# Kernel optimization log

Measured on AMD Instinct MI355X. Metric: run time of the kernel, lower is better.

## Reference

```python
import jax, jax.numpy as jnp
import numpy as np

B, C, O, H, W = 4, 256, 256, 64, 64
KH = KW = 3
KK = KH * KW
PAD = 1  # stride=1, padding=1 -> output spatial == input spatial


def setup_inputs() -> dict:
    key = jax.random.key(0)
    k0, k1, k2, k3 = jax.random.split(key, 4)
    x = jax.random.normal(k0, (B, C, H, W), jnp.float32)
    # offset-predicting conv: small weights -> realistic sub-pixel offsets
    w_off = jax.random.normal(k1, (3 * KK, C, KH, KW), jnp.float32) * 0.01
    b_off = jnp.zeros((3 * KK,), jnp.float32)
    w_def = jax.random.normal(k2, (O, C, KH, KW), jnp.float32) * (1.0 / np.sqrt(C * KK))
    b_def = jax.random.normal(k3, (O,), jnp.float32) * 0.01
    return {"x": x, "w_off": w_off, "b_off": b_off, "w_def": w_def, "b_def": b_def}


def _conv2d(x, w, b):
    y = jax.lax.conv_general_dilated(
        x, w, window_strides=(1, 1), padding=((PAD, PAD), (PAD, PAD)),
        dimension_numbers=("NCHW", "OIHW", "NCHW"))
    return y + b[None, :, None, None]


def _deform_conv2d(x, offsets, mask, w, b):
    # torchvision modulated DeformConv2d, stride=1, pad=1, dilation=1.
    Bx, Cx, Hx, Wx = x.shape
    Ox = w.shape[0]
    # offsets: [B, 2*KK, H, W] with channel 2k = dy, 2k+1 = dx for tap k
    off = offsets.reshape(Bx, KK, 2, Hx, Wx)
    ky, kx = jnp.meshgrid(jnp.arange(KH), jnp.arange(KW), indexing="ij")
    ky = ky.reshape(KK)
    kx = kx.reshape(KK)
    base_y = (ky[:, None, None] - PAD + jnp.arange(Hx)[None, :, None]).astype(x.dtype)  # [KK,H,1]
    base_x = (kx[:, None, None] - PAD + jnp.arange(Wx)[None, None, :]).astype(x.dtype)  # [KK,1,W]
    sy = off[:, :, 0] + base_y  # [B,KK,H,W] sample rows
    sx = off[:, :, 1] + base_x  # [B,KK,H,W] sample cols

    y0 = jnp.floor(sy)
    x0 = jnp.floor(sx)
    ty = sy - y0  # fractional weights (grad flows to offsets through these)
    tx = sx - x0

    x_flat = x.reshape(Bx, Cx, Hx * Wx)
    val = jnp.zeros((Bx, Cx, KK, Hx, Wx), x.dtype)
    for dy in (0, 1):  # 4 bilinear corners (fixed small loop)
        for dx in (0, 1):
            yi = y0.astype(jnp.int32) + dy
            xi = x0.astype(jnp.int32) + dx
            wgt = (ty if dy else 1.0 - ty) * (tx if dx else 1.0 - tx)
            valid = (yi >= 0) & (yi < Hx) & (xi >= 0) & (xi < Wx)  # zero outside
            idx = (jnp.clip(yi, 0, Hx - 1) * Wx + jnp.clip(xi, 0, Wx - 1)).reshape(Bx, 1, -1)
            g = jnp.take_along_axis(x_flat, idx, axis=2).reshape(Bx, Cx, KK, Hx, Wx)
            val = val + g * jnp.where(valid, wgt, 0.0)[:, None]

    val = val * mask.reshape(Bx, 1, KK, Hx, Wx)  # modulation
    out = jnp.einsum("bckhw,ock->bohw", val, w.reshape(Ox, Cx, KK))
    return out + b[None, :, None, None]


def reference(x, w_off, b_off, w_def, b_def):
    pred = _conv2d(x, w_off, b_off)            # [B, 3*KK, H, W]
    offsets = pred[:, : 2 * KK]                # [B, 2*KK, H, W]
    mask = jax.nn.sigmoid(pred[:, 2 * KK:])    # [B, KK, H, W]
    return _deform_conv2d(x, offsets, mask, w_def, b_def)
```

## Files before the change

### kernel.cpp

```cpp
#include <hip/hip_runtime.h>

#define BB 4
#define CCH 256
#define OCH 256
#define HH 64
#define WW 64
#define HWSZ 4096

typedef __bf16 bf16_t;
typedef bf16_t bf16x8 __attribute__((ext_vector_type(8)));
typedef float f32x4 __attribute__((ext_vector_type(4)));

__device__ __forceinline__ unsigned int bpack(float a, float b) {
    unsigned int ua = __float_as_uint(a);
    ua = (ua + 0x7FFFu + ((ua >> 16) & 1u)) >> 16;
    unsigned int ub = __float_as_uint(b);
    ub = (ub + 0x7FFFu + ((ub >> 16) & 1u)) >> 16;
    return ua | (ub << 16);
}
__device__ __forceinline__ float blo(unsigned int u) { return __uint_as_float(u << 16); }
__device__ __forceinline__ float bhi(unsigned int u) { return __uint_as_float(u & 0xFFFF0000u); }

__global__ __launch_bounds__(256) void k_xT(const float* __restrict__ x,
                                            ushort* __restrict__ xT) {
    int b = blockIdx.x >> 6;
    int h = blockIdx.x & 63;
    int tid = threadIdx.x;
    int wv = tid >> 6;
    int lane = tid & 63;

    __shared__ unsigned int buf[64][130];

    const float* xp = x + ((size_t)b * CCH + wv * 64) * HWSZ + h * WW + lane;
#pragma unroll 8
    for (int i = 0; i < 32; ++i) {
        float a = xp[(size_t)(2 * i) * HWSZ];
        float c = xp[(size_t)(2 * i + 1) * HWSZ];
        buf[lane][wv * 32 + i] = bpack(a, c);
    }
    __syncthreads();

    ushort* dst = xT + ((size_t)(b * 64 + h) * 64) * 256;
#pragma unroll
    for (int r = 0; r < 16; ++r) {
        int idx = tid + r * 256;
        int w = idx >> 6;
        int q = idx & 63;
        uint2 v = *(const uint2*)&buf[w][2 * q];
        *(uint2*)(dst + (size_t)w * 256 + q * 4) = v;
    }
}

__global__ void k_prep(const float* __restrict__ w_off, const float* __restrict__ w_def,
                       const float* __restrict__ b_def,
                       ushort* __restrict__ w1F, ushort* __restrict__ w2F,
                       float* __restrict__ P, float* __restrict__ out) {
    int i = blockIdx.x * blockDim.x + threadIdx.x;
    if (i < 73728) {
        int j = i & 7;
        int o = (i >> 3) & 31;
        int cSub = (i >> 8) & 31;
        int k = i >> 13;
        float v = 0.0f;
        if (o < 27) v = w_off[((size_t)o * CCH + cSub * 8 + j) * 9 + k];
        unsigned int u = __float_as_uint(v);
        u = (u + 0x7FFFu + ((u >> 16) & 1u)) >> 16;
        w1F[i] = (ushort)u;
        return;
    }
    i -= 73728;
    if (i < 589824) {
        int j = i & 7;
        int o = (i >> 3) & 255;
        int cg = (i >> 11) & 31;
        int k = i >> 16;
        float v = w_def[(size_t)o * 2304 + (cg * 8 + j) * 9 + k];
        unsigned int u = __float_as_uint(v);
        u = (u + 0x7FFFu + ((u >> 16) & 1u)) >> 16;
        w2F[i] = (ushort)u;
        return;
    }
    i -= 589824;
    if (i < 110592) {
        ((float4*)P)[i] = make_float4(0.f, 0.f, 0.f, 0.f);
        return;
    }
    i -= 110592;
    if (i < 1048576) {
        float v = b_def[(i >> 10) & 255];
        ((float4*)out)[i] = make_float4(v, v, v, v);
    }
}

__global__ __launch_bounds__(256) void k_pred3(const ushort* __restrict__ xT,
                                               const ushort* __restrict__ w1F,
                                               float* __restrict__ P) {
    int bid = blockIdx.x;
    int L = (bid & 7) * 128 + (bid >> 3);
    int g = L & 3;
    int h = (L >> 2) & 63;
    int b = L >> 8;
    int tid = threadIdx.x;
    int spx  = tid & 63;
    int sgrp = tid >> 6;
    int lane = tid & 63;
    int wv   = tid >> 6;
    int l16  = lane & 15;
    int lq   = lane >> 4;

    __shared__ ushort b_lds[2][4][4][16][8];

    const ushort* xTb = xT + (size_t)b * HWSZ * 256;
    const bf16x8* w1v = (const bf16x8*)w1F;

    f32x4 acc[2];
    acc[0] = (f32x4){0.f, 0.f, 0.f, 0.f};
    acc[1] = (f32x4){0.f, 0.f, 0.f, 0.f};

    auto stage = [&](int t, int buf) {
        int cg = 2 * g + (t >= 9);
        int k = t - (t >= 9 ? 9 : 0);
        int y   = h + k / 3 - 1;
        int pxs = spx + k % 3 - 1;
        bool ok = (y >= 0 && y < HH && pxs >= 0 && pxs < WW);
        uint4 v = make_uint4(0u, 0u, 0u, 0u);
        if (ok) v = *(const uint4*)(xTb + (size_t)(y * WW + pxs) * 256 + cg * 32 + sgrp * 8);
        *(uint4*)&b_lds[buf][sgrp][spx >> 4][spx & 15][0] = v;
    };

    stage(0, 0);
    __syncthreads();

    for (int t = 0; t < 18; ++t) {
        int cur = t & 1;
        int cg = 2 * g + (t >= 9);
        int k  = t - (t >= 9 ? 9 : 0);
        int row = k * 32 + cg * 4 + lq;
        bf16x8 a0 = w1v[(size_t)row * 32 + 0 * 16 + l16];
        bf16x8 a1 = w1v[(size_t)row * 32 + 1 * 16 + l16];
        if (t < 17) stage(t + 1, cur ^ 1);
        bf16x8 bfrag = *(const bf16x8*)&b_lds[cur][lq][wv][l16][0];
        acc[0] = __builtin_amdgcn_mfma_f32_16x16x32_bf16(a0, bfrag, acc[0], 0, 0, 0);
        acc[1] = __builtin_amdgcn_mfma_f32_16x16x32_bf16(a1, bfrag, acc[1], 0, 0, 0);
        __syncthreads();
    }

#pragma unroll
    for (int mf = 0; mf < 2; ++mf) {
#pragma unroll
        for (int r = 0; r < 4; ++r) {
            int o = mf * 16 + lq * 4 + r;
            if (o < 27) {
                atomicAdd(&P[((size_t)b * 27 + o) * HWSZ + h * WW + wv * 16 + l16],
                          acc[mf][r]);
            }
        }
    }
}

__global__ __launch_bounds__(512, 4) void k_deform8(const ushort* __restrict__ xT,
                                                    const float* __restrict__ P,
                                                    const float* __restrict__ b_off,
                                                    const ushort* __restrict__ w2F,
                                                    float* __restrict__ out) {
    int bid = blockIdx.x;
    int L = (bid & 7) * 64 + (bid >> 3);
    int cs = L & 1;
    int h  = (L >> 1) & 63;
    int b  = L >> 7;
    int tid = threadIdx.x;
    int lane = tid & 63;
    int wv   = tid >> 6;
    int l16  = lane & 15;
    int lq   = lane >> 4;
    int px   = tid >> 3;
    int cl   = tid & 7;

    __shared__ ushort b_lds[2][8][4][16][8];

    const char* xTc = (const char*)xT + (size_t)b * HWSZ * 512 + cs * 256 + cl * 16;
    const bf16x8* w2b = (const bf16x8*)w2F + (size_t)(cs * 16) * 256 + wv * 32 + l16;

    uint4* wdst0 = (uint4*)&b_lds[0][cl][px >> 4][(px & 15) ^ cl][0];
    uint4* wdst1 = (uint4*)&b_lds[1][cl][px >> 4][(px & 15) ^ cl][0];

    f32x4 acc[2][4];
#pragma unroll
    for (int mf = 0; mf < 2; ++mf)
#pragma unroll
        for (int nt = 0; nt < 4; ++nt) acc[mf][nt] = (f32x4){0.f, 0.f, 0.f, 0.f};

    const float* Pb = P + (size_t)b * 27 * HWSZ + h * WW + px;

    float pOy, pOx, pMr, bOy, bOx, bMr;
    float wgt[4];
    const char* aptr[4];

    auto loadP = [&](int k) {
        pOy = Pb[(size_t)(2 * k) * HWSZ];
        pOx = Pb[(size_t)(2 * k + 1) * HWSZ];
        pMr = Pb[(size_t)(18 + k) * HWSZ];
        bOy = b_off[2 * k];
        bOx = b_off[2 * k + 1];
        bMr = b_off[18 + k];
    };
    auto calcDesc = [&](int k) {
        float offy = pOy + bOy;
        float offx = pOx + bOx;
        float m = 1.0f / (1.0f + expf(-(pMr + bMr)));
        float sy = offy + (float)(h + k / 3 - 1);
        float sx = offx + (float)(px + k % 3 - 1);
        float y0f = floorf(sy), x0f = floorf(sx);
        float ty = sy - y0f, tx = sx - x0f;
        int y0 = (int)y0f, x0 = (int)x0f;
#pragma unroll
        for (int dy = 0; dy < 2; ++dy) {
#pragma unroll
            for (int dx = 0; dx < 2; ++dx) {
                int yi = y0 + dy, xi = x0 + dx;
                bool ok = (yi >= 0 && yi < HH && xi >= 0 && xi < WW);
                float wg = (dy ? ty : 1.0f - ty) * (dx ? tx : 1.0f - tx) * m;
                wgt[dy * 2 + dx]  = ok ? wg : 0.0f;
                aptr[dy * 2 + dx] = xTc + (size_t)(ok ? (yi * WW + xi) : 0) * 512;
            }
        }
    };

    uint4 gbA[4], gbB[4];
    float wgtA[4], wgtB[4];
    bf16x8 aA[2][2], aB[2][2];

    auto issueGatherTo = [&](uint4 (&gb)[4], float (&wg)[4], int off) {
#pragma unroll
        for (int c = 0; c < 4; ++c) gb[c] = *(const uint4*)(aptr[c] + off);
#pragma unroll
        for (int c = 0; c < 4; ++c) wg[c] = wgt[c];
    };
    auto combineFrom = [&](const uint4 (&g)[4], const float (&w)[4]) -> uint4 {
        uint4 r;
        {
            float lo = w[0]*blo(g[0].x) + w[1]*blo(g[1].x) + w[2]*blo(g[2].x) + w[3]*blo(g[3].x);
            float hi = w[0]*bhi(g[0].x) + w[1]*bhi(g[1].x) + w[2]*bhi(g[2].x) + w[3]*bhi(g[3].x);
            r.x = bpack(lo, hi);
        }
        {
            float lo = w[0]*blo(g[0].y) + w[1]*blo(g[1].y) + w[2]*blo(g[2].y) + w[3]*blo(g[3].y);
            float hi = w[0]*bhi(g[0].y) + w[1]*bhi(g[1].y) + w[2]*bhi(g[2].y) + w[3]*bhi(g[3].y);
            r.y = bpack(lo, hi);
        }
        {
            float lo = w[0]*blo(g[0].z) + w[1]*blo(g[1].z) + w[2]*blo(g[2].z) + w[3]*blo(g[3].z);
            float hi = w[0]*bhi(g[0].z) + w[1]*bhi(g[1].z) + w[2]*bhi(g[2].z) + w[3]*bhi(g[3].z);
            r.z = bpack(lo, hi);
        }
        {
            float lo = w[0]*blo(g[0].w) + w[1]*blo(g[1].w) + w[2]*blo(g[2].w) + w[3]*blo(g[3].w);
            float hi = w[0]*bhi(g[0].w) + w[1]*bhi(g[1].w) + w[2]*bhi(g[2].w) + w[3]*bhi(g[3].w);
            r.w = bpack(lo, hi);
        }
        return r;
    };
    auto loadATo = [&](bf16x8 (&a)[2][2], int t) {
        size_t base = ((size_t)((t >> 1) * 32 + (t & 1) * 8) + lq) * 256;
#pragma unroll
        for (int g = 0; g < 2; ++g)
#pragma unroll
            for (int mf = 0; mf < 2; ++mf)
                a[mf][g] = w2b[base + (size_t)g * 1024 + mf * 16];
    };

#define MFMA_BODY(BUF, AREG)                                                        \
    do {                                                                            \
        bf16x8 bfr[2][4];                                                           \
        _Pragma("unroll")                                                           \
        for (int g = 0; g < 2; ++g) {                                               \
            int kg = g * 4 + lq;                                                    \
            _Pragma("unroll")                                                       \
            for (int nt = 0; nt < 4; ++nt)                                          \
                bfr[g][nt] = *(const bf16x8*)&b_lds[BUF][kg][nt][l16 ^ kg][0];      \
        }                                                                           \
        _Pragma("unroll")                                                           \
        for (int g = 0; g < 2; ++g)                                                 \
            _Pragma("unroll")                                                       \
            for (int mf = 0; mf < 2; ++mf)                                          \
                _Pragma("unroll")                                                   \
                for (int nt = 0; nt < 4; ++nt)                                      \
                    acc[mf][nt] = __builtin_amdgcn_mfma_f32_16x16x32_bf16(          \
                        AREG[mf][g], bfr[g][nt], acc[mf][nt], 0, 0, 0);             \
    } while (0)

    loadP(0);
    calcDesc(0);
    issueGatherTo(gbA, wgtA, 0);
    issueGatherTo(gbB, wgtB, 128);
    loadP(1);
    loadATo(aA, 0);
    *wdst0 = combineFrom(gbA, wgtA);
    __syncthreads();

    for (int tp = 0; tp < 9; ++tp) {
        if (tp < 8) {
            calcDesc(tp + 1);
            issueGatherTo(gbA, wgtA, 0);
        }
        loadATo(aB, 2 * tp + 1);
        MFMA_BODY(0, aA);
        *wdst1 = combineFrom(gbB, wgtB);
        __syncthreads();

        if (tp < 8) {
            issueGatherTo(gbB, wgtB, 128);
            if (tp < 7) loadP(tp + 2);
            loadATo(aA, 2 * tp + 2);
        }
        MFMA_BODY(1, aB);
        if (tp < 8) {
            *wdst0 = combineFrom(gbA, wgtA);
        }
        __syncthreads();
    }
#undef MFMA_BODY

#pragma unroll
    for (int mf = 0; mf < 2; ++mf) {
#pragma unroll
        for (int nt = 0; nt < 4; ++nt) {
#pragma unroll
            for (int r = 0; r < 4; ++r) {
                int o = wv * 32 + mf * 16 + lq * 4 + r;
                atomicAdd(&out[((size_t)b * OCH + o) * HWSZ + h * WW + nt * 16 + l16],
                          acc[mf][nt][r]);
            }
        }
    }
}

extern "C" void kernel_launch(void* const* d_in, const int* in_sizes, int n_in,
                              void* d_out, int out_size, void* d_ws, size_t ws_size,
                              hipStream_t stream) {
    const float* x     = (const float*)d_in[0];
    const float* w_off = (const float*)d_in[1];
    const float* b_off = (const float*)d_in[2];
    const float* w_def = (const float*)d_in[3];
    const float* b_def = (const float*)d_in[4];
    float* out = (float*)d_out;

    float*  P   = (float*)d_ws;
    ushort* w1F = (ushort*)(P + (size_t)BB * 27 * HWSZ);
    ushort* w2F = w1F + 73728;
    ushort* xT  = w2F + 589824;

    hipLaunchKernelGGL(k_prep, dim3(7120), dim3(256), 0, stream,
                       w_off, w_def, b_def, w1F, w2F, P, out);
    hipLaunchKernelGGL(k_xT, dim3(BB * HH), dim3(256), 0, stream, x, xT);
    hipLaunchKernelGGL(k_pred3, dim3(1024), dim3(256), 0, stream, xT, w1F, P);
    hipLaunchKernelGGL(k_deform8, dim3(512), dim3(512), 0, stream, xT, P, b_off, w2F, out);
}
```

Measured before the change: 89.90 us.

## Merge transpose into prep kernel, use hardware bf16 convert, lighter barriers

Folds the x-transpose kernel into the prep kernel as its first 256 blocks, removing one launch. Replaces the manual bit-twiddling bf16 rounding with the compiler's native bf16 conversion. Swaps __syncthreads for a barrier that waits only on LDS counters, so global loads in flight are not drained. Reorders the pipelines so the global gather is issued before the MFMAs and the LDS store comes after (pred) or before (deform). The lighter barrier relies on no global-memory ordering being needed across it, and the native convert may round NaN or other edge cases differently.

```diff
diff --git a/kernel.cpp b/kernel.cpp
--- a/kernel.cpp
+++ b/kernel.cpp
@@ -9,53 +9,65 @@
 
 typedef __bf16 bf16_t;
 typedef bf16_t bf16x8 __attribute__((ext_vector_type(8)));
+typedef bf16_t bf16x2_t __attribute__((ext_vector_type(2)));
 typedef float f32x4 __attribute__((ext_vector_type(4)));
 
-__device__ __forceinline__ unsigned int bpack(float a, float b) {
-    unsigned int ua = __float_as_uint(a);
-    ua = (ua + 0x7FFFu + ((ua >> 16) & 1u)) >> 16;
-    unsigned int ub = __float_as_uint(b);
-    ub = (ub + 0x7FFFu + ((ub >> 16) & 1u)) >> 16;
-    return ua | (ub << 16);
+__device__ __forceinline__ unsigned int packbf(float a, float b) {
+    bf16x2_t p;
+    p.x = (__bf16)a;
+    p.y = (__bf16)b;
+    return __builtin_bit_cast(unsigned int, p);
 }
 __device__ __forceinline__ float blo(unsigned int u) { return __uint_as_float(u << 16); }
 __device__ __forceinline__ float bhi(unsigned int u) { return __uint_as_float(u & 0xFFFF0000u); }
 
-__global__ __launch_bounds__(256) void k_xT(const float* __restrict__ x,
-                                            ushort* __restrict__ xT) {
-    int b = blockIdx.x >> 6;
-    int h = blockIdx.x & 63;
-    int tid = threadIdx.x;
-    int wv = tid >> 6;
-    int lane = tid & 63;
-
-    __shared__ unsigned int buf[64][130];
-
-    const float* xp = x + ((size_t)b * CCH + wv * 64) * HWSZ + h * WW + lane;
+__device__ __forceinline__ void block_sync() {
+    asm volatile("s_waitcnt lgkmcnt(0)" ::: "memory");
+    __builtin_amdgcn_s_barrier();
+    __builtin_amdgcn_sched_barrier(0);
+}
+
+__global__ __launch_bounds__(256) void k_prep(const float* __restrict__ x,
+                                              const float* __restrict__ w_off,
+                                              const float* __restrict__ w_def,
+                                              const float* __restrict__ b_def,
+                                              ushort* __restrict__ xT,
+                                              ushort* __restrict__ w1F,
+                                              ushort* __restrict__ w2F,
+                                              float* __restrict__ P,
+                                              float* __restrict__ out) {
+    int bid = blockIdx.x;
+    if (bid < 256) {
+        int b = bid >> 6;
+        int h = bid & 63;
+        int tid = threadIdx.x;
+        int wv = tid >> 6;
+        int lane = tid & 63;
+
+        __shared__ unsigned int buf[64][130];
+
+        const float* xp = x + ((size_t)b * CCH + wv * 64) * HWSZ + h * WW + lane;
 #pragma unroll 8
-    for (int i = 0; i < 32; ++i) {
-        float a = xp[(size_t)(2 * i) * HWSZ];
-        float c = xp[(size_t)(2 * i + 1) * HWSZ];
-        buf[lane][wv * 32 + i] = bpack(a, c);
-    }
-    __syncthreads();
-
-    ushort* dst = xT + ((size_t)(b * 64 + h) * 64) * 256;
-#pragma unroll
-    for (int r = 0; r < 16; ++r) {
-        int idx = tid + r * 256;
-        int w = idx >> 6;
-        int q = idx & 63;
-        uint2 v = *(const uint2*)&buf[w][2 * q];
-        *(uint2*)(dst + (size_t)w * 256 + q * 4) = v;
-    }
-}
-
-__global__ void k_prep(const float* __restrict__ w_off, const float* __restrict__ w_def,
-                       const float* __restrict__ b_def,
-                       ushort* __restrict__ w1F, ushort* __restrict__ w2F,
-                       float* __restrict__ P, float* __restrict__ out) {
-    int i = blockIdx.x * blockDim.x + threadIdx.x;
+        for (int i = 0; i < 32; ++i) {
+            float a = xp[(size_t)(2 * i) * HWSZ];
+            float c = xp[(size_t)(2 * i + 1) * HWSZ];
+            buf[lane][wv * 32 + i] = packbf(a, c);
+        }
+        __syncthreads();
+
+        ushort* dst = xT + ((size_t)(b * 64 + h) * 64) * 256;
+#pragma unroll
+        for (int r = 0; r < 16; ++r) {
+            int idx = tid + r * 256;
+            int w = idx >> 6;
+            int q = idx & 63;
+            uint2 v = *(const uint2*)&buf[w][2 * q];
+            *(uint2*)(dst + (size_t)w * 256 + q * 4) = v;
+        }
+        return;
+    }
+
+    int i = (bid - 256) * 256 + threadIdx.x;
     if (i < 73728) {
         int j = i & 7;
         int o = (i >> 3) & 31;
@@ -63,9 +75,7 @@
         int k = i >> 13;
         float v = 0.0f;
         if (o < 27) v = w_off[((size_t)o * CCH + cSub * 8 + j) * 9 + k];
-        unsigned int u = __float_as_uint(v);
-        u = (u + 0x7FFFu + ((u >> 16) & 1u)) >> 16;
-        w1F[i] = (ushort)u;
+        w1F[i] = (ushort)(packbf(v, 0.f) & 0xFFFFu);
         return;
     }
     i -= 73728;
@@ -75,9 +85,7 @@
         int cg = (i >> 11) & 31;
         int k = i >> 16;
         float v = w_def[(size_t)o * 2304 + (cg * 8 + j) * 9 + k];
-        unsigned int u = __float_as_uint(v);
-        u = (u + 0x7FFFu + ((u >> 16) & 1u)) >> 16;
-        w2F[i] = (ushort)u;
+        w2F[i] = (ushort)(packbf(v, 0.f) & 0xFFFFu);
         return;
     }
     i -= 589824;
@@ -117,7 +125,7 @@
     acc[0] = (f32x4){0.f, 0.f, 0.f, 0.f};
     acc[1] = (f32x4){0.f, 0.f, 0.f, 0.f};
 
-    auto stage = [&](int t, int buf) {
+    auto stageLoad = [&](int t) -> uint4 {
         int cg = 2 * g + (t >= 9);
         int k = t - (t >= 9 ? 9 : 0);
         int y   = h + k / 3 - 1;
@@ -125,24 +133,32 @@
         bool ok = (y >= 0 && y < HH && pxs >= 0 && pxs < WW);
         uint4 v = make_uint4(0u, 0u, 0u, 0u);
         if (ok) v = *(const uint4*)(xTb + (size_t)(y * WW + pxs) * 256 + cg * 32 + sgrp * 8);
+        return v;
+    };
+    auto stageWrite = [&](uint4 v, int buf) {
         *(uint4*)&b_lds[buf][sgrp][spx >> 4][spx & 15][0] = v;
     };
 
-    stage(0, 0);
-    __syncthreads();
+    {
+        uint4 g0 = stageLoad(0);
+        stageWrite(g0, 0);
+    }
+    block_sync();
 
     for (int t = 0; t < 18; ++t) {
         int cur = t & 1;
+        uint4 gN;
+        if (t < 17) gN = stageLoad(t + 1);
         int cg = 2 * g + (t >= 9);
         int k  = t - (t >= 9 ? 9 : 0);
         int row = k * 32 + cg * 4 + lq;
         bf16x8 a0 = w1v[(size_t)row * 32 + 0 * 16 + l16];
         bf16x8 a1 = w1v[(size_t)row * 32 + 1 * 16 + l16];
-        if (t < 17) stage(t + 1, cur ^ 1);
         bf16x8 bfrag = *(const bf16x8*)&b_lds[cur][lq][wv][l16][0];
         acc[0] = __builtin_amdgcn_mfma_f32_16x16x32_bf16(a0, bfrag, acc[0], 0, 0, 0);
         acc[1] = __builtin_amdgcn_mfma_f32_16x16x32_bf16(a1, bfrag, acc[1], 0, 0, 0);
-        __syncthreads();
+        if (t < 17) stageWrite(gN, cur ^ 1);
+        block_sync();
     }
 
 #pragma unroll
@@ -158,7 +174,7 @@
     }
 }
 
-__global__ __launch_bounds__(512, 4) void k_deform8(const ushort* __restrict__ xT,
+__global__ __launch_bounds__(512, 4) void k_deform9(const ushort* __restrict__ xT,
                                                     const float* __restrict__ P,
                                                     const float* __restrict__ b_off,
                                                     const ushort* __restrict__ w2F,
@@ -241,22 +257,22 @@
         {
             float lo = w[0]*blo(g[0].x) + w[1]*blo(g[1].x) + w[2]*blo(g[2].x) + w[3]*blo(g[3].x);
             float hi = w[0]*bhi(g[0].x) + w[1]*bhi(g[1].x) + w[2]*bhi(g[2].x) + w[3]*bhi(g[3].x);
-            r.x = bpack(lo, hi);
+            r.x = packbf(lo, hi);
         }
         {
             float lo = w[0]*blo(g[0].y) + w[1]*blo(g[1].y) + w[2]*blo(g[2].y) + w[3]*blo(g[3].y);
             float hi = w[0]*bhi(g[0].y) + w[1]*bhi(g[1].y) + w[2]*bhi(g[2].y) + w[3]*bhi(g[3].y);
-            r.y = bpack(lo, hi);
+            r.y = packbf(lo, hi);
         }
         {
             float lo = w[0]*blo(g[0].z) + w[1]*blo(g[1].z) + w[2]*blo(g[2].z) + w[3]*blo(g[3].z);
             float hi = w[0]*bhi(g[0].z) + w[1]*bhi(g[1].z) + w[2]*bhi(g[2].z) + w[3]*bhi(g[3].z);
-            r.z = bpack(lo, hi);
+            r.z = packbf(lo, hi);
         }
         {
             float lo = w[0]*blo(g[0].w) + w[1]*blo(g[1].w) + w[2]*blo(g[2].w) + w[3]*blo(g[3].w);
             float hi = w[0]*bhi(g[0].w) + w[1]*bhi(g[1].w) + w[2]*bhi(g[2].w) + w[3]*bhi(g[3].w);
-            r.w = bpack(lo, hi);
+            r.w = packbf(lo, hi);
         }
         return r;
     };
@@ -296,7 +312,7 @@
     loadP(1);
     loadATo(aA, 0);
     *wdst0 = combineFrom(gbA, wgtA);
-    __syncthreads();
+    block_sync();
 
     for (int tp = 0; tp < 9; ++tp) {
         if (tp < 8) {
@@ -304,20 +320,18 @@
             issueGatherTo(gbA, wgtA, 0);
         }
         loadATo(aB, 2 * tp + 1);
+        *wdst1 = combineFrom(gbB, wgtB);
         MFMA_BODY(0, aA);
-        *wdst1 = combineFrom(gbB, wgtB);
-        __syncthreads();
+        block_sync();
 
         if (tp < 8) {
             issueGatherTo(gbB, wgtB, 128);
             if (tp < 7) loadP(tp + 2);
             loadATo(aA, 2 * tp + 2);
+            *wdst0 = combineFrom(gbA, wgtA);
         }
         MFMA_BODY(1, aB);
-        if (tp < 8) {
-            *wdst0 = combineFrom(gbA, wgtA);
-        }
-        __syncthreads();
+        block_sync();
     }
 #undef MFMA_BODY
 
@@ -350,9 +364,8 @@
     ushort* w2F = w1F + 73728;
     ushort* xT  = w2F + 589824;
 
-    hipLaunchKernelGGL(k_prep, dim3(7120), dim3(256), 0, stream,
-                       w_off, w_def, b_def, w1F, w2F, P, out);
-    hipLaunchKernelGGL(k_xT, dim3(BB * HH), dim3(256), 0, stream, x, xT);
+    hipLaunchKernelGGL(k_prep, dim3(7376), dim3(256), 0, stream,
+                       x, w_off, w_def, b_def, xT, w1F, w2F, P, out);
     hipLaunchKernelGGL(k_pred3, dim3(1024), dim3(256), 0, stream, xT, w1F, P);
-    hipLaunchKernelGGL(k_deform8, dim3(512), dim3(512), 0, stream, xT, P, b_off, w2F, out);
-}
+    hipLaunchKernelGGL(k_deform9, dim3(512), dim3(512), 0, stream, xT, P, b_off, w2F, out);
+}
```

New measurement: 95.18 us. +5.9%, slower.
